# Performance work log

Hardware: AMD Instinct MI355X
Metric: run time of the kernel (lower is better)

Reference implementation:

```python
import jax, jax.numpy as jnp
import numpy as np

B, D, H, T = 2048, 16, 256, 50
BETA_MIN, BETA_MAX = 0.1, 20.0


def setup_inputs() -> dict:
    key = jax.random.key(0)
    ks = jax.random.split(key, 6)
    s1 = 1.0 / np.sqrt(D)
    s2 = 1.0 / np.sqrt(H)
    return {
        "x": jax.random.normal(ks[0], (B, D), dtype=jnp.float32),
        "W1": jax.random.normal(ks[1], (D, H), dtype=jnp.float32) * s1,
        "b1": jnp.zeros((H,), dtype=jnp.float32),
        "wt": jax.random.normal(ks[2], (H,), dtype=jnp.float32) * 0.1,
        "W2": jax.random.normal(ks[3], (H, D), dtype=jnp.float32) * s2,
        "b2": jnp.zeros((D,), dtype=jnp.float32),
    }


def _dynamics(x, t, W1, b1, wt, W2, b2):
    # Reverse-time probability-flow ODE drift for a VP-SDE:
    #   dx/dt = f(x,t) - 0.5 * g(t)^2 * score(x,t)
    # with f = -0.5*beta(t)*x, g^2 = beta(t), score = MLP(x, t).
    beta = BETA_MIN + t * (BETA_MAX - BETA_MIN)
    h = jnp.tanh(x @ W1 + t * wt + b1)  # [B, H]
    score = h @ W2 + b2                 # [B, D]
    return -0.5 * beta * (x + score)


def _trace_jac(f, x):
    # Exact per-sample trace of the [D, D] Jacobian of f (batched over B)
    # via D forward-mode JVPs with basis tangents (batched, no per-output loop).
    eye = jnp.eye(x.shape[-1], dtype=x.dtype)

    def jvp_col(e):
        _, jv = jax.jvp(f, (x,), (jnp.broadcast_to(e, x.shape),))
        return jv  # [B, D]

    cols = jax.vmap(jvp_col)(eye)       # [D, B, D]
    return jnp.einsum("ibi->b", cols)   # sum of Jacobian diagonal per sample


def reference(x, W1, b1, wt, W2, b2):
    times = jnp.linspace(1e-3, 1.0, T, dtype=jnp.float32)

    def F(xc, t):
        dyn = lambda y: _dynamics(y, t, W1, b1, wt, W2, b2)
        dx = dyn(xc)
        tr = _trace_jac(dyn, xc)
        return dx, tr

    def rk4_step(carry, ts):
        xc, ldj = carry
        t0, t1 = ts
        h = t1 - t0
        k1x, k1t = F(xc, t0)
        k2x, k2t = F(xc + 0.5 * h * k1x, t0 + 0.5 * h)
        k3x, k3t = F(xc + 0.5 * h * k2x, t0 + 0.5 * h)
        k4x, k4t = F(xc + h * k3x, t1)
        xn = xc + (h / 6.0) * (k1x + 2.0 * k2x + 2.0 * k3x + k4x)
        ln = ldj + (h / 6.0) * (k1t + 2.0 * k2t + 2.0 * k3t + k4t)
        return (xn, ln), (xn, ln)

    ldj0 = jnp.zeros((x.shape[0],), dtype=x.dtype)
    (xf, ldjf), (xs, _) = jax.lax.scan(
        rk4_step, (x, ldj0), (times[:-1], times[1:])
    )
    xt = jnp.concatenate([x[None], xs], axis=0)  # [T, B, D] trajectory
    return xf, ldjf, xt
```

## Files before the change

### kernel.cpp

```cpp
#include <hip/hip_runtime.h>
#include <stdint.h>


typedef _Float16 f16x2 __attribute__((ext_vector_type(2)));

#if defined(__has_builtin)
#if __has_builtin(__builtin_amdgcn_fdot2)
#define HAVE_FDOT2 1
#endif
#endif

__device__ __forceinline__ float fdot2f(f16x2 a, f16x2 b, float c) {
#ifdef HAVE_FDOT2
    return __builtin_amdgcn_fdot2(a, b, c, false);
#else
    return fmaf((float)a.y, (float)b.y, fmaf((float)a.x, (float)b.x, c));
#endif
}

__device__ __forceinline__ uint32_t pk(float a, float b) {
    f16x2 v; v.x = (_Float16)a; v.y = (_Float16)b;
    return __builtin_bit_cast(uint32_t, v);
}
__device__ __forceinline__ f16x2 upk(uint32_t u) {
    return __builtin_bit_cast(f16x2, u);
}

#define DPP_XOR1 0xB1
#define DPP_XOR2 0x4E
#define DPP_RHM  0x141
template <int CTRL>
__device__ __forceinline__ float dpp_add(float x) {
    int v = __builtin_amdgcn_update_dpp(
        0, __builtin_bit_cast(int, x), CTRL, 0xF, 0xF, true);
    return x + __builtin_bit_cast(float, v);
}

#define Bn 2048
#define Dn 16
#define Hn 256
#define Tn 50
#define CH 20

__global__ __launch_bounds__(64) void ode_kernel(
    const float* __restrict__ x_in,
    const float* __restrict__ W1,
    const float* __restrict__ b1v,
    const float* __restrict__ wtv,
    const float* __restrict__ W2,
    const float* __restrict__ b2v,
    float* __restrict__ out)
{
    __shared__ __align__(16) uint32_t h_lds[8 * CH];

    const int L  = threadIdx.x;
    const int g8 = L >> 3;
    const int c  = L & 7;
    const int ia = 2 * g8, ib = ia + 1;
    const int k0 = 4 * L;
    const int gs = blockIdx.x;

    const float K2 = 2.88539008f;

    f16x2 w1p[4][8];
    float b1k[4], wtk[4], ck[4];
    #pragma unroll
    for (int q = 0; q < 4; ++q) {
        const int k = k0 + q;
        #pragma unroll
        for (int j = 0; j < 8; ++j) {
            f16x2 v;
            v.x = (_Float16)(K2 * W1[(2 * j)     * Hn + k]);
            v.y = (_Float16)(K2 * W1[(2 * j + 1) * Hn + k]);
            w1p[q][j] = v;
        }
        b1k[q] = K2 * b1v[k];
        wtk[q] = K2 * wtv[k];
        float s = 0.f;
        #pragma unroll
        for (int ii = 0; ii < 16; ++ii)
            s = fmaf(W1[ii * Hn + k], W2[k * Dn + ii], s);
        ck[q] = s;
    }
    f16x2 w2a[16], w2b[16];
    #pragma unroll
    for (int m = 0; m < 16; ++m) {
        f16x2 va, vb;
        va.x = (_Float16)W2[(32 * c + 2 * m)     * Dn + ia];
        va.y = (_Float16)W2[(32 * c + 2 * m + 1) * Dn + ia];
        vb.x = (_Float16)W2[(32 * c + 2 * m)     * Dn + ib];
        vb.y = (_Float16)W2[(32 * c + 2 * m + 1) * Dn + ib];
        w2a[m] = va; w2b[m] = vb;
    }
    const float b2a = b2v[ia], b2b = b2v[ib];

    float xa = x_in[gs * Dn + ia];
    float xb = x_in[gs * Dn + ib];
    float ldjl  = 0.f;
    float wbsum = 0.f;

    float* xf_out  = out;
    float* ldj_out = out + (size_t)Bn * Dn;
    float* xt_ptr  = out + (size_t)Bn * Dn + Bn + gs * Dn + ia;

    if (c == 0) *(float2*)xt_ptr = make_float2(xa, xb);
    xt_ptr += Bn * Dn;

    const int hwidx = CH * (L >> 3) + 2 * (L & 7);

    uint32_t se0, se1, se2, se3, se4, se5, se6, se7;
    auto bcast = [&](float ea, float eb) {
        const uint32_t vpk = pk(ea, eb);
        se0 = __builtin_amdgcn_readlane(vpk,  0);
        se1 = __builtin_amdgcn_readlane(vpk,  8);
        se2 = __builtin_amdgcn_readlane(vpk, 16);
        se3 = __builtin_amdgcn_readlane(vpk, 24);
        se4 = __builtin_amdgcn_readlane(vpk, 32);
        se5 = __builtin_amdgcn_readlane(vpk, 40);
        se6 = __builtin_amdgcn_readlane(vpk, 48);
        se7 = __builtin_amdgcn_readlane(vpk, 56);
    };

    auto Feval = [&](float xeva, float xevb, float tt, float wgt,
                     float& dxa, float& dxb) {
        const f16x2 xp[8] = { upk(se0), upk(se1), upk(se2), upk(se3),
                              upk(se4), upk(se5), upk(se6), upk(se7) };
        float u0 = fmaf(tt, wtk[0], b1k[0]);
        float u1 = fmaf(tt, wtk[1], b1k[1]);
        float u2 = fmaf(tt, wtk[2], b1k[2]);
        float u3 = fmaf(tt, wtk[3], b1k[3]);
        #pragma unroll
        for (int j = 0; j < 8; ++j) {
            u0 = fdot2f(xp[j], w1p[0][j], u0);
            u1 = fdot2f(xp[j], w1p[1][j], u1);
            u2 = fdot2f(xp[j], w1p[2][j], u2);
            u3 = fdot2f(xp[j], w1p[3][j], u3);
        }
        const float h0 = fmaf(-2.f, __builtin_amdgcn_rcpf(__builtin_amdgcn_exp2f(u0) + 1.f), 1.f);
        const float h1 = fmaf(-2.f, __builtin_amdgcn_rcpf(__builtin_amdgcn_exp2f(u1) + 1.f), 1.f);
        const float h2 = fmaf(-2.f, __builtin_amdgcn_rcpf(__builtin_amdgcn_exp2f(u2) + 1.f), 1.f);
        const float h3 = fmaf(-2.f, __builtin_amdgcn_rcpf(__builtin_amdgcn_exp2f(u3) + 1.f), 1.f);
        *(uint2*)&h_lds[hwidx] = make_uint2(pk(h0, h1), pk(h2, h3));

        const float gl = (fmaf(-h0 * h0, ck[0], ck[0]) + fmaf(-h1 * h1, ck[1], ck[1]))
                       + (fmaf(-h2 * h2, ck[2], ck[2]) + fmaf(-h3 * h3, ck[3], ck[3]));
        const float beta = fmaf(tt, 19.9f, 0.1f);
        const float nhb  = -0.5f * beta;
        const float wb   = wgt * nhb;
        ldjl  = fmaf(wb, gl, ldjl);
        wbsum += wb;

        asm volatile("" ::: "memory");

        float sa0 = 0.f, sa1 = 0.f, sb0 = 0.f, sb1 = 0.f;
        #pragma unroll
        for (int mq = 0; mq < 4; ++mq) {
            const uint4 hv = *(const uint4*)&h_lds[CH * c + 4 * mq];
            const f16x2 p0 = upk(hv.x), p1 = upk(hv.y), p2 = upk(hv.z), p3 = upk(hv.w);
            sa0 = fdot2f(p0, w2a[4 * mq + 0], sa0);
            sb0 = fdot2f(p0, w2b[4 * mq + 0], sb0);
            sa1 = fdot2f(p1, w2a[4 * mq + 1], sa1);
            sb1 = fdot2f(p1, w2b[4 * mq + 1], sb1);
            sa0 = fdot2f(p2, w2a[4 * mq + 2], sa0);
            sb0 = fdot2f(p2, w2b[4 * mq + 2], sb0);
            sa1 = fdot2f(p3, w2a[4 * mq + 3], sa1);
            sb1 = fdot2f(p3, w2b[4 * mq + 3], sb1);
        }
        float sca = sa0 + sa1, scb = sb0 + sb1;
        sca = dpp_add<DPP_XOR1>(sca);  scb = dpp_add<DPP_XOR1>(scb);
        sca = dpp_add<DPP_XOR2>(sca);  scb = dpp_add<DPP_XOR2>(scb);
        sca = dpp_add<DPP_RHM >(sca);  scb = dpp_add<DPP_RHM >(scb);
        sca += b2a;  scb += b2b;

        dxa = nhb * (xeva + sca);
        dxb = nhb * (xevb + scb);
    };

    const float t_lo = 1e-3f;
    const float dt   = (1.0f - 1e-3f) / (float)(Tn - 1);
    const float hh   = dt;
    const float w1w  = hh * (1.f / 6.f);
    const float w2w  = hh * (2.f / 6.f);

    bcast(xa, xb);
    for (int j = 0; j < Tn - 1; ++j) {
        const float t0 = fmaf((float)j, dt, t_lo);
        const float tm = t0 + 0.5f * hh;
        const float t1 = t0 + hh;
        float k1a, k1b, k2a, k2b, k3a, k3b, k4a, k4b;

        Feval(xa, xb, t0, w1w, k1a, k1b);
        const float e2a = fmaf(0.5f * hh, k1a, xa);
        const float e2b = fmaf(0.5f * hh, k1b, xb);
        bcast(e2a, e2b);
        Feval(e2a, e2b, tm, w2w, k2a, k2b);
        const float e3a = fmaf(0.5f * hh, k2a, xa);
        const float e3b = fmaf(0.5f * hh, k2b, xb);
        bcast(e3a, e3b);
        Feval(e3a, e3b, tm, w2w, k3a, k3b);
        const float e4a = fmaf(hh, k3a, xa);
        const float e4b = fmaf(hh, k3b, xb);
        bcast(e4a, e4b);
        Feval(e4a, e4b, t1, w1w, k4a, k4b);

        xa = fmaf(w1w, k1a + 2.f * (k2a + k3a) + k4a, xa);
        xb = fmaf(w1w, k1b + 2.f * (k2b + k3b) + k4b, xb);
        if (c == 0) *(float2*)xt_ptr = make_float2(xa, xb);
        xt_ptr += Bn * Dn;
        bcast(xa, xb);
    }

    if (c == 0) *(float2*)(xf_out + gs * Dn + ia) = make_float2(xa, xb);

    ldjl = fmaf(0.25f, wbsum, ldjl);
    #pragma unroll
    for (int off = 1; off < 64; off <<= 1)
        ldjl += __shfl_xor(ldjl, off);
    if (L == 0) ldj_out[gs] = ldjl;
}

extern "C" void kernel_launch(void* const* d_in, const int* in_sizes, int n_in,
                              void* d_out, int out_size, void* d_ws, size_t ws_size,
                              hipStream_t stream) {
    const float* x  = (const float*)d_in[0];
    const float* W1 = (const float*)d_in[1];
    const float* b1 = (const float*)d_in[2];
    const float* wt = (const float*)d_in[3];
    const float* W2 = (const float*)d_in[4];
    const float* b2 = (const float*)d_in[5];
    (void)in_sizes; (void)n_in; (void)out_size; (void)d_ws; (void)ws_size;
    ode_kernel<<<Bn, 64, 0, stream>>>(x, W1, b1, wt, W2, b2, (float*)d_out);
}
```

Before: 171.6 us.

## Switch fp16 dot2 math to packed fp32 FMA with 4-output-per-lane layout

Replaces the fp16 fdot2 arithmetic for both MLP layers with packed fp32 v_pk_fma operations. Hidden activations are now kept in LDS as fp32. The second-layer work is remapped so each lane owns 4 output dims over 16 hidden chunks instead of 2 dims over 8 chunks, which needs one extra DPP reduction stage. This improves accuracy but doubles LDS traffic and register footprint, and packed fp32 FMA may give lower throughput than fp16 dot2 on this latency-bound, one-wave-per-sample kernel.

```diff
diff --git a/kernel.cpp b/kernel.cpp
--- a/kernel.cpp
+++ b/kernel.cpp
@@ -2,38 +2,26 @@
 #include <stdint.h>
 
 
-typedef _Float16 f16x2 __attribute__((ext_vector_type(2)));
-
-#if defined(__has_builtin)
-#if __has_builtin(__builtin_amdgcn_fdot2)
-#define HAVE_FDOT2 1
-#endif
-#endif
-
-__device__ __forceinline__ float fdot2f(f16x2 a, f16x2 b, float c) {
-#ifdef HAVE_FDOT2
-    return __builtin_amdgcn_fdot2(a, b, c, false);
-#else
-    return fmaf((float)a.y, (float)b.y, fmaf((float)a.x, (float)b.x, c));
-#endif
-}
-
-__device__ __forceinline__ uint32_t pk(float a, float b) {
-    f16x2 v; v.x = (_Float16)a; v.y = (_Float16)b;
-    return __builtin_bit_cast(uint32_t, v);
-}
-__device__ __forceinline__ f16x2 upk(uint32_t u) {
-    return __builtin_bit_cast(f16x2, u);
-}
-
-#define DPP_XOR1 0xB1
-#define DPP_XOR2 0x4E
-#define DPP_RHM  0x141
+typedef float v2f __attribute__((ext_vector_type(2)));
+
+__device__ __forceinline__ v2f fma2(v2f a, v2f b, v2f c) {
+    return __builtin_elementwise_fma(a, b, c);
+}
+
+#define DPP_X1  0xB1
+#define DPP_X2  0x4E
+#define DPP_HM  0x141
+#define DPP_MIR 0x140
 template <int CTRL>
 __device__ __forceinline__ float dpp_add(float x) {
-    int v = __builtin_amdgcn_update_dpp(
-        0, __builtin_bit_cast(int, x), CTRL, 0xF, 0xF, true);
+    const int xi = __builtin_bit_cast(int, x);
+    const int v  = __builtin_amdgcn_update_dpp(xi, xi, CTRL, 0xF, 0xF, false);
     return x + __builtin_bit_cast(float, v);
+}
+
+__device__ __forceinline__ float rlf(float v, int l) {
+    return __builtin_bit_cast(
+        float, __builtin_amdgcn_readlane(__builtin_bit_cast(int, v), l));
 }
 
 #define Bn 2048
@@ -51,28 +39,28 @@
     const float* __restrict__ b2v,
     float* __restrict__ out)
 {
-    __shared__ __align__(16) uint32_t h_lds[8 * CH];
+    __shared__ __align__(16) float h_lds[16 * CH];
 
     const int L  = threadIdx.x;
-    const int g8 = L >> 3;
-    const int c  = L & 7;
-    const int ia = 2 * g8, ib = ia + 1;
+    const int iq = L >> 4;
+    const int c4 = L & 15;
+    const int i0 = 4 * iq;
     const int k0 = 4 * L;
     const int gs = blockIdx.x;
 
     const float K2 = 2.88539008f;
 
-    f16x2 w1p[4][8];
+    v2f w1v[4][8];
     float b1k[4], wtk[4], ck[4];
     #pragma unroll
     for (int q = 0; q < 4; ++q) {
         const int k = k0 + q;
         #pragma unroll
         for (int j = 0; j < 8; ++j) {
-            f16x2 v;
-            v.x = (_Float16)(K2 * W1[(2 * j)     * Hn + k]);
-            v.y = (_Float16)(K2 * W1[(2 * j + 1) * Hn + k]);
-            w1p[q][j] = v;
+            v2f v;
+            v.x = K2 * W1[(2 * j)     * Hn + k];
+            v.y = K2 * W1[(2 * j + 1) * Hn + k];
+            w1v[q][j] = v;
         }
         b1k[q] = K2 * b1v[k];
         wtk[q] = K2 * wtv[k];
@@ -82,65 +70,62 @@
             s = fmaf(W1[ii * Hn + k], W2[k * Dn + ii], s);
         ck[q] = s;
     }
-    f16x2 w2a[16], w2b[16];
-    #pragma unroll
-    for (int m = 0; m < 16; ++m) {
-        f16x2 va, vb;
-        va.x = (_Float16)W2[(32 * c + 2 * m)     * Dn + ia];
-        va.y = (_Float16)W2[(32 * c + 2 * m + 1) * Dn + ia];
-        vb.x = (_Float16)W2[(32 * c + 2 * m)     * Dn + ib];
-        vb.y = (_Float16)W2[(32 * c + 2 * m + 1) * Dn + ib];
-        w2a[m] = va; w2b[m] = vb;
-    }
-    const float b2a = b2v[ia], b2b = b2v[ib];
-
-    float xa = x_in[gs * Dn + ia];
-    float xb = x_in[gs * Dn + ib];
-    float ldjl  = 0.f;
-    float wbsum = 0.f;
+    v2f w2v[4][8];
+    #pragma unroll
+    for (int q = 0; q < 4; ++q)
+        #pragma unroll
+        for (int n = 0; n < 8; ++n) {
+            v2f v;
+            v.x = W2[(16 * c4 + 2 * n)     * Dn + i0 + q];
+            v.y = W2[(16 * c4 + 2 * n + 1) * Dn + i0 + q];
+            w2v[q][n] = v;
+        }
+    float b2q[4];
+    #pragma unroll
+    for (int q = 0; q < 4; ++q) b2q[q] = b2v[i0 + q];
+
+    const float4 xld = *(const float4*)(x_in + gs * Dn + i0);
+    float x0 = xld.x, x1 = xld.y, x2 = xld.z, x3 = xld.w;
+    float ldjl = 0.f, wbsum = 0.f;
 
     float* xf_out  = out;
     float* ldj_out = out + (size_t)Bn * Dn;
-    float* xt_ptr  = out + (size_t)Bn * Dn + Bn + gs * Dn + ia;
-
-    if (c == 0) *(float2*)xt_ptr = make_float2(xa, xb);
+    float* xt_ptr  = out + (size_t)Bn * Dn + Bn + gs * Dn + i0;
+
+    if (c4 == 0) *(float4*)xt_ptr = make_float4(x0, x1, x2, x3);
     xt_ptr += Bn * Dn;
 
-    const int hwidx = CH * (L >> 3) + 2 * (L & 7);
-
-    uint32_t se0, se1, se2, se3, se4, se5, se6, se7;
-    auto bcast = [&](float ea, float eb) {
-        const uint32_t vpk = pk(ea, eb);
-        se0 = __builtin_amdgcn_readlane(vpk,  0);
-        se1 = __builtin_amdgcn_readlane(vpk,  8);
-        se2 = __builtin_amdgcn_readlane(vpk, 16);
-        se3 = __builtin_amdgcn_readlane(vpk, 24);
-        se4 = __builtin_amdgcn_readlane(vpk, 32);
-        se5 = __builtin_amdgcn_readlane(vpk, 40);
-        se6 = __builtin_amdgcn_readlane(vpk, 48);
-        se7 = __builtin_amdgcn_readlane(vpk, 56);
+    v2f xv[8];
+    auto bcast = [&](float e0, float e1, float e2, float e3) {
+        #pragma unroll
+        for (int j = 0; j < 4; ++j) {
+            v2f a, b;
+            a.x = rlf(e0, 16 * j);  a.y = rlf(e1, 16 * j);
+            b.x = rlf(e2, 16 * j);  b.y = rlf(e3, 16 * j);
+            xv[2 * j]     = a;
+            xv[2 * j + 1] = b;
+        }
     };
 
-    auto Feval = [&](float xeva, float xevb, float tt, float wgt,
-                     float& dxa, float& dxb) {
-        const f16x2 xp[8] = { upk(se0), upk(se1), upk(se2), upk(se3),
-                              upk(se4), upk(se5), upk(se6), upk(se7) };
-        float u0 = fmaf(tt, wtk[0], b1k[0]);
-        float u1 = fmaf(tt, wtk[1], b1k[1]);
-        float u2 = fmaf(tt, wtk[2], b1k[2]);
-        float u3 = fmaf(tt, wtk[3], b1k[3]);
+    auto Feval = [&](float e0, float e1, float e2, float e3, float tt, float wgt,
+                     float& d0, float& d1, float& d2, float& d3) {
+        v2f a0 = {0.f, 0.f}, a1 = {0.f, 0.f}, a2 = {0.f, 0.f}, a3 = {0.f, 0.f};
         #pragma unroll
         for (int j = 0; j < 8; ++j) {
-            u0 = fdot2f(xp[j], w1p[0][j], u0);
-            u1 = fdot2f(xp[j], w1p[1][j], u1);
-            u2 = fdot2f(xp[j], w1p[2][j], u2);
-            u3 = fdot2f(xp[j], w1p[3][j], u3);
-        }
+            a0 = fma2(xv[j], w1v[0][j], a0);
+            a1 = fma2(xv[j], w1v[1][j], a1);
+            a2 = fma2(xv[j], w1v[2][j], a2);
+            a3 = fma2(xv[j], w1v[3][j], a3);
+        }
+        const float u0 = fmaf(tt, wtk[0], b1k[0]) + (a0.x + a0.y);
+        const float u1 = fmaf(tt, wtk[1], b1k[1]) + (a1.x + a1.y);
+        const float u2 = fmaf(tt, wtk[2], b1k[2]) + (a2.x + a2.y);
+        const float u3 = fmaf(tt, wtk[3], b1k[3]) + (a3.x + a3.y);
         const float h0 = fmaf(-2.f, __builtin_amdgcn_rcpf(__builtin_amdgcn_exp2f(u0) + 1.f), 1.f);
         const float h1 = fmaf(-2.f, __builtin_amdgcn_rcpf(__builtin_amdgcn_exp2f(u1) + 1.f), 1.f);
         const float h2 = fmaf(-2.f, __builtin_amdgcn_rcpf(__builtin_amdgcn_exp2f(u2) + 1.f), 1.f);
         const float h3 = fmaf(-2.f, __builtin_amdgcn_rcpf(__builtin_amdgcn_exp2f(u3) + 1.f), 1.f);
-        *(uint2*)&h_lds[hwidx] = make_uint2(pk(h0, h1), pk(h2, h3));
+        *(float4*)&h_lds[CH * (L >> 2) + 4 * (L & 3)] = make_float4(h0, h1, h2, h3);
 
         const float gl = (fmaf(-h0 * h0, ck[0], ck[0]) + fmaf(-h1 * h1, ck[1], ck[1]))
                        + (fmaf(-h2 * h2, ck[2], ck[2]) + fmaf(-h3 * h3, ck[3], ck[3]));
@@ -152,28 +137,33 @@
 
         asm volatile("" ::: "memory");
 
-        float sa0 = 0.f, sa1 = 0.f, sb0 = 0.f, sb1 = 0.f;
-        #pragma unroll
-        for (int mq = 0; mq < 4; ++mq) {
-            const uint4 hv = *(const uint4*)&h_lds[CH * c + 4 * mq];
-            const f16x2 p0 = upk(hv.x), p1 = upk(hv.y), p2 = upk(hv.z), p3 = upk(hv.w);
-            sa0 = fdot2f(p0, w2a[4 * mq + 0], sa0);
-            sb0 = fdot2f(p0, w2b[4 * mq + 0], sb0);
-            sa1 = fdot2f(p1, w2a[4 * mq + 1], sa1);
-            sb1 = fdot2f(p1, w2b[4 * mq + 1], sb1);
-            sa0 = fdot2f(p2, w2a[4 * mq + 2], sa0);
-            sb0 = fdot2f(p2, w2b[4 * mq + 2], sb0);
-            sa1 = fdot2f(p3, w2a[4 * mq + 3], sa1);
-            sb1 = fdot2f(p3, w2b[4 * mq + 3], sb1);
-        }
-        float sca = sa0 + sa1, scb = sb0 + sb1;
-        sca = dpp_add<DPP_XOR1>(sca);  scb = dpp_add<DPP_XOR1>(scb);
-        sca = dpp_add<DPP_XOR2>(sca);  scb = dpp_add<DPP_XOR2>(scb);
-        sca = dpp_add<DPP_RHM >(sca);  scb = dpp_add<DPP_RHM >(scb);
-        sca += b2a;  scb += b2b;
-
-        dxa = nhb * (xeva + sca);
-        dxb = nhb * (xevb + scb);
+        const float* hb = &h_lds[CH * c4];
+        v2f s0 = {0.f, 0.f}, s1 = {0.f, 0.f}, s2 = {0.f, 0.f}, s3 = {0.f, 0.f};
+        #pragma unroll
+        for (int m = 0; m < 4; ++m) {
+            const float4 hp = *(const float4*)(hb + 4 * m);
+            v2f hA; hA.x = hp.x; hA.y = hp.y;
+            v2f hB; hB.x = hp.z; hB.y = hp.w;
+            s0 = fma2(hA, w2v[0][2 * m], s0);  s0 = fma2(hB, w2v[0][2 * m + 1], s0);
+            s1 = fma2(hA, w2v[1][2 * m], s1);  s1 = fma2(hB, w2v[1][2 * m + 1], s1);
+            s2 = fma2(hA, w2v[2][2 * m], s2);  s2 = fma2(hB, w2v[2][2 * m + 1], s2);
+            s3 = fma2(hA, w2v[3][2 * m], s3);  s3 = fma2(hB, w2v[3][2 * m + 1], s3);
+        }
+        float t0 = s0.x + s0.y, t1 = s1.x + s1.y;
+        float t2 = s2.x + s2.y, t3 = s3.x + s3.y;
+        t0 = dpp_add<DPP_X1 >(t0); t1 = dpp_add<DPP_X1 >(t1);
+        t2 = dpp_add<DPP_X1 >(t2); t3 = dpp_add<DPP_X1 >(t3);
+        t0 = dpp_add<DPP_X2 >(t0); t1 = dpp_add<DPP_X2 >(t1);
+        t2 = dpp_add<DPP_X2 >(t2); t3 = dpp_add<DPP_X2 >(t3);
+        t0 = dpp_add<DPP_HM >(t0); t1 = dpp_add<DPP_HM >(t1);
+        t2 = dpp_add<DPP_HM >(t2); t3 = dpp_add<DPP_HM >(t3);
+        t0 = dpp_add<DPP_MIR>(t0); t1 = dpp_add<DPP_MIR>(t1);
+        t2 = dpp_add<DPP_MIR>(t2); t3 = dpp_add<DPP_MIR>(t3);
+
+        d0 = nhb * (e0 + t0 + b2q[0]);
+        d1 = nhb * (e1 + t1 + b2q[1]);
+        d2 = nhb * (e2 + t2 + b2q[2]);
+        d3 = nhb * (e3 + t3 + b2q[3]);
     };
 
     const float t_lo = 1e-3f;
@@ -182,35 +172,37 @@
     const float w1w  = hh * (1.f / 6.f);
     const float w2w  = hh * (2.f / 6.f);
 
-    bcast(xa, xb);
+    bcast(x0, x1, x2, x3);
     for (int j = 0; j < Tn - 1; ++j) {
         const float t0 = fmaf((float)j, dt, t_lo);
         const float tm = t0 + 0.5f * hh;
         const float t1 = t0 + hh;
-        float k1a, k1b, k2a, k2b, k3a, k3b, k4a, k4b;
-
-        Feval(xa, xb, t0, w1w, k1a, k1b);
-        const float e2a = fmaf(0.5f * hh, k1a, xa);
-        const float e2b = fmaf(0.5f * hh, k1b, xb);
-        bcast(e2a, e2b);
-        Feval(e2a, e2b, tm, w2w, k2a, k2b);
-        const float e3a = fmaf(0.5f * hh, k2a, xa);
-        const float e3b = fmaf(0.5f * hh, k2b, xb);
-        bcast(e3a, e3b);
-        Feval(e3a, e3b, tm, w2w, k3a, k3b);
-        const float e4a = fmaf(hh, k3a, xa);
-        const float e4b = fmaf(hh, k3b, xb);
-        bcast(e4a, e4b);
-        Feval(e4a, e4b, t1, w1w, k4a, k4b);
-
-        xa = fmaf(w1w, k1a + 2.f * (k2a + k3a) + k4a, xa);
-        xb = fmaf(w1w, k1b + 2.f * (k2b + k3b) + k4b, xb);
-        if (c == 0) *(float2*)xt_ptr = make_float2(xa, xb);
+        float k1[4], k2[4], k3[4], k4[4];
+
+        Feval(x0, x1, x2, x3, t0, w1w, k1[0], k1[1], k1[2], k1[3]);
+        float e0 = fmaf(0.5f * hh, k1[0], x0), e1 = fmaf(0.5f * hh, k1[1], x1);
+        float e2 = fmaf(0.5f * hh, k1[2], x2), e3 = fmaf(0.5f * hh, k1[3], x3);
+        bcast(e0, e1, e2, e3);
+        Feval(e0, e1, e2, e3, tm, w2w, k2[0], k2[1], k2[2], k2[3]);
+        e0 = fmaf(0.5f * hh, k2[0], x0); e1 = fmaf(0.5f * hh, k2[1], x1);
+        e2 = fmaf(0.5f * hh, k2[2], x2); e3 = fmaf(0.5f * hh, k2[3], x3);
+        bcast(e0, e1, e2, e3);
+        Feval(e0, e1, e2, e3, tm, w2w, k3[0], k3[1], k3[2], k3[3]);
+        e0 = fmaf(hh, k3[0], x0); e1 = fmaf(hh, k3[1], x1);
+        e2 = fmaf(hh, k3[2], x2); e3 = fmaf(hh, k3[3], x3);
+        bcast(e0, e1, e2, e3);
+        Feval(e0, e1, e2, e3, t1, w1w, k4[0], k4[1], k4[2], k4[3]);
+
+        x0 = fmaf(w1w, k1[0] + 2.f * (k2[0] + k3[0]) + k4[0], x0);
+        x1 = fmaf(w1w, k1[1] + 2.f * (k2[1] + k3[1]) + k4[1], x1);
+        x2 = fmaf(w1w, k1[2] + 2.f * (k2[2] + k3[2]) + k4[2], x2);
+        x3 = fmaf(w1w, k1[3] + 2.f * (k2[3] + k3[3]) + k4[3], x3);
+        if (c4 == 0) *(float4*)xt_ptr = make_float4(x0, x1, x2, x3);
         xt_ptr += Bn * Dn;
-        bcast(xa, xb);
+        bcast(x0, x1, x2, x3);
     }
 
-    if (c == 0) *(float2*)(xf_out + gs * Dn + ia) = make_float2(xa, xb);
+    if (c4 == 0) *(float4*)(xf_out + gs * Dn + i0) = make_float4(x0, x1, x2, x3);
 
     ldjl = fmaf(0.25f, wbsum, ldjl);
     #pragma unroll
```

Measured after the change: 208.0 us. +21.2%, slower.

## Split each sample's hidden dimension across two wavefronts with LDS exchange

Applied to the files above, without the earlier changes.

Each block now uses 128 threads (two wavefronts) per sample instead of one. Each wave handles half of the 256 hidden units, which halves the per-thread W1/W2 register footprint and the fdot2 work. Partial score sums are exchanged through a double-buffered LDS array with a __syncthreads per function evaluation. The DPP reduction also changes to keep the old value on invalid lanes. In exchange the latency-bound serial chain gains 200 block barriers and extra LDS traffic, while total wave count doubles to 4096.

```diff
diff --git a/kernel.cpp b/kernel.cpp
--- a/kernel.cpp
+++ b/kernel.cpp
@@ -26,13 +26,13 @@
     return __builtin_bit_cast(f16x2, u);
 }
 
-#define DPP_XOR1 0xB1
-#define DPP_XOR2 0x4E
-#define DPP_RHM  0x141
+#define DPP_X1  0xB1
+#define DPP_X2  0x4E
+#define DPP_HM  0x141
 template <int CTRL>
 __device__ __forceinline__ float dpp_add(float x) {
-    int v = __builtin_amdgcn_update_dpp(
-        0, __builtin_bit_cast(int, x), CTRL, 0xF, 0xF, true);
+    const int xi = __builtin_bit_cast(int, x);
+    const int v  = __builtin_amdgcn_update_dpp(xi, xi, CTRL, 0xF, 0xF, false);
     return x + __builtin_bit_cast(float, v);
 }
 
@@ -40,9 +40,8 @@
 #define Dn 16
 #define Hn 256
 #define Tn 50
-#define CH 20
-
-__global__ __launch_bounds__(64) void ode_kernel(
+
+__global__ __launch_bounds__(128, 4) void ode_kernel(
     const float* __restrict__ x_in,
     const float* __restrict__ W1,
     const float* __restrict__ b1v,
@@ -51,22 +50,26 @@
     const float* __restrict__ b2v,
     float* __restrict__ out)
 {
-    __shared__ __align__(16) uint32_t h_lds[8 * CH];
-
-    const int L  = threadIdx.x;
+    __shared__ uint32_t h_lds[128];
+    __shared__ float    sc_buf[2][2][16];
+    __shared__ float    ldj_buf[2];
+
+    const int t  = threadIdx.x;
+    const int W  = t >> 6;
+    const int L  = t & 63;
     const int g8 = L >> 3;
     const int c  = L & 7;
     const int ia = 2 * g8, ib = ia + 1;
-    const int k0 = 4 * L;
+    const int kp = 64 * W + L;
     const int gs = blockIdx.x;
 
     const float K2 = 2.88539008f;
 
-    f16x2 w1p[4][8];
-    float b1k[4], wtk[4], ck[4];
+    f16x2 w1p[2][8];
+    float b1k[2], wtk[2], ck[2];
     #pragma unroll
-    for (int q = 0; q < 4; ++q) {
-        const int k = k0 + q;
+    for (int q = 0; q < 2; ++q) {
+        const int k = 2 * kp + q;
         #pragma unroll
         for (int j = 0; j < 8; ++j) {
             f16x2 v;
@@ -82,31 +85,30 @@
             s = fmaf(W1[ii * Hn + k], W2[k * Dn + ii], s);
         ck[q] = s;
     }
-    f16x2 w2a[16], w2b[16];
+    f16x2 w2a[8], w2b[8];
     #pragma unroll
-    for (int m = 0; m < 16; ++m) {
+    for (int m = 0; m < 8; ++m) {
+        const int kk = 128 * W + 16 * c + 2 * m;
         f16x2 va, vb;
-        va.x = (_Float16)W2[(32 * c + 2 * m)     * Dn + ia];
-        va.y = (_Float16)W2[(32 * c + 2 * m + 1) * Dn + ia];
-        vb.x = (_Float16)W2[(32 * c + 2 * m)     * Dn + ib];
-        vb.y = (_Float16)W2[(32 * c + 2 * m + 1) * Dn + ib];
+        va.x = (_Float16)W2[kk * Dn + ia];  va.y = (_Float16)W2[(kk + 1) * Dn + ia];
+        vb.x = (_Float16)W2[kk * Dn + ib];  vb.y = (_Float16)W2[(kk + 1) * Dn + ib];
         w2a[m] = va; w2b[m] = vb;
     }
     const float b2a = b2v[ia], b2b = b2v[ib];
 
     float xa = x_in[gs * Dn + ia];
     float xb = x_in[gs * Dn + ib];
-    float ldjl  = 0.f;
-    float wbsum = 0.f;
+    float ldjl = 0.f, wbsum = 0.f;
 
     float* xf_out  = out;
     float* ldj_out = out + (size_t)Bn * Dn;
     float* xt_ptr  = out + (size_t)Bn * Dn + Bn + gs * Dn + ia;
 
-    if (c == 0) *(float2*)xt_ptr = make_float2(xa, xb);
+    if (W == 0 && c == 0) *(float2*)xt_ptr = make_float2(xa, xb);
     xt_ptr += Bn * Dn;
 
-    const int hwidx = CH * (L >> 3) + 2 * (L & 7);
+    const int hwr = 64 * W + L;
+    const int hrd = 64 * W + 8 * c;
 
     uint32_t se0, se1, se2, se3, se4, se5, se6, se7;
     auto bcast = [&](float ea, float eb) {
@@ -121,29 +123,31 @@
         se7 = __builtin_amdgcn_readlane(vpk, 56);
     };
 
+    int fe = 0;
+
     auto Feval = [&](float xeva, float xevb, float tt, float wgt,
                      float& dxa, float& dxb) {
-        const f16x2 xp[8] = { upk(se0), upk(se1), upk(se2), upk(se3),
-                              upk(se4), upk(se5), upk(se6), upk(se7) };
+        const int p = fe & 1; ++fe;
+
         float u0 = fmaf(tt, wtk[0], b1k[0]);
         float u1 = fmaf(tt, wtk[1], b1k[1]);
-        float u2 = fmaf(tt, wtk[2], b1k[2]);
-        float u3 = fmaf(tt, wtk[3], b1k[3]);
-        #pragma unroll
-        for (int j = 0; j < 8; ++j) {
-            u0 = fdot2f(xp[j], w1p[0][j], u0);
-            u1 = fdot2f(xp[j], w1p[1][j], u1);
-            u2 = fdot2f(xp[j], w1p[2][j], u2);
-            u3 = fdot2f(xp[j], w1p[3][j], u3);
+        {
+            const f16x2 xp0 = upk(se0), xp1 = upk(se1), xp2 = upk(se2), xp3 = upk(se3);
+            const f16x2 xp4 = upk(se4), xp5 = upk(se5), xp6 = upk(se6), xp7 = upk(se7);
+            u0 = fdot2f(xp0, w1p[0][0], u0);  u1 = fdot2f(xp0, w1p[1][0], u1);
+            u0 = fdot2f(xp1, w1p[0][1], u0);  u1 = fdot2f(xp1, w1p[1][1], u1);
+            u0 = fdot2f(xp2, w1p[0][2], u0);  u1 = fdot2f(xp2, w1p[1][2], u1);
+            u0 = fdot2f(xp3, w1p[0][3], u0);  u1 = fdot2f(xp3, w1p[1][3], u1);
+            u0 = fdot2f(xp4, w1p[0][4], u0);  u1 = fdot2f(xp4, w1p[1][4], u1);
+            u0 = fdot2f(xp5, w1p[0][5], u0);  u1 = fdot2f(xp5, w1p[1][5], u1);
+            u0 = fdot2f(xp6, w1p[0][6], u0);  u1 = fdot2f(xp6, w1p[1][6], u1);
+            u0 = fdot2f(xp7, w1p[0][7], u0);  u1 = fdot2f(xp7, w1p[1][7], u1);
         }
         const float h0 = fmaf(-2.f, __builtin_amdgcn_rcpf(__builtin_amdgcn_exp2f(u0) + 1.f), 1.f);
         const float h1 = fmaf(-2.f, __builtin_amdgcn_rcpf(__builtin_amdgcn_exp2f(u1) + 1.f), 1.f);
-        const float h2 = fmaf(-2.f, __builtin_amdgcn_rcpf(__builtin_amdgcn_exp2f(u2) + 1.f), 1.f);
-        const float h3 = fmaf(-2.f, __builtin_amdgcn_rcpf(__builtin_amdgcn_exp2f(u3) + 1.f), 1.f);
-        *(uint2*)&h_lds[hwidx] = make_uint2(pk(h0, h1), pk(h2, h3));
-
-        const float gl = (fmaf(-h0 * h0, ck[0], ck[0]) + fmaf(-h1 * h1, ck[1], ck[1]))
-                       + (fmaf(-h2 * h2, ck[2], ck[2]) + fmaf(-h3 * h3, ck[3], ck[3]));
+        h_lds[hwr] = pk(h0, h1);
+
+        const float gl   = fmaf(-h0 * h0, ck[0], ck[0]) + fmaf(-h1 * h1, ck[1], ck[1]);
         const float beta = fmaf(tt, 19.9f, 0.1f);
         const float nhb  = -0.5f * beta;
         const float wb   = wgt * nhb;
@@ -152,28 +156,29 @@
 
         asm volatile("" ::: "memory");
 
-        float sa0 = 0.f, sa1 = 0.f, sb0 = 0.f, sb1 = 0.f;
-        #pragma unroll
-        for (int mq = 0; mq < 4; ++mq) {
-            const uint4 hv = *(const uint4*)&h_lds[CH * c + 4 * mq];
-            const f16x2 p0 = upk(hv.x), p1 = upk(hv.y), p2 = upk(hv.z), p3 = upk(hv.w);
-            sa0 = fdot2f(p0, w2a[4 * mq + 0], sa0);
-            sb0 = fdot2f(p0, w2b[4 * mq + 0], sb0);
-            sa1 = fdot2f(p1, w2a[4 * mq + 1], sa1);
-            sb1 = fdot2f(p1, w2b[4 * mq + 1], sb1);
-            sa0 = fdot2f(p2, w2a[4 * mq + 2], sa0);
-            sb0 = fdot2f(p2, w2b[4 * mq + 2], sb0);
-            sa1 = fdot2f(p3, w2a[4 * mq + 3], sa1);
-            sb1 = fdot2f(p3, w2b[4 * mq + 3], sb1);
-        }
-        float sca = sa0 + sa1, scb = sb0 + sb1;
-        sca = dpp_add<DPP_XOR1>(sca);  scb = dpp_add<DPP_XOR1>(scb);
-        sca = dpp_add<DPP_XOR2>(sca);  scb = dpp_add<DPP_XOR2>(scb);
-        sca = dpp_add<DPP_RHM >(sca);  scb = dpp_add<DPP_RHM >(scb);
-        sca += b2a;  scb += b2b;
-
-        dxa = nhb * (xeva + sca);
-        dxb = nhb * (xevb + scb);
+        const uint4 hv0 = *(const uint4*)&h_lds[hrd];
+        const uint4 hv1 = *(const uint4*)&h_lds[hrd + 4];
+        const f16x2 p0 = upk(hv0.x), p1 = upk(hv0.y), p2 = upk(hv0.z), p3 = upk(hv0.w);
+        const f16x2 p4 = upk(hv1.x), p5 = upk(hv1.y), p6 = upk(hv1.z), p7 = upk(hv1.w);
+        float sa = 0.f, sb = 0.f;
+        sa = fdot2f(p0, w2a[0], sa);  sb = fdot2f(p0, w2b[0], sb);
+        sa = fdot2f(p1, w2a[1], sa);  sb = fdot2f(p1, w2b[1], sb);
+        sa = fdot2f(p2, w2a[2], sa);  sb = fdot2f(p2, w2b[2], sb);
+        sa = fdot2f(p3, w2a[3], sa);  sb = fdot2f(p3, w2b[3], sb);
+        sa = fdot2f(p4, w2a[4], sa);  sb = fdot2f(p4, w2b[4], sb);
+        sa = fdot2f(p5, w2a[5], sa);  sb = fdot2f(p5, w2b[5], sb);
+        sa = fdot2f(p6, w2a[6], sa);  sb = fdot2f(p6, w2b[6], sb);
+        sa = fdot2f(p7, w2a[7], sa);  sb = fdot2f(p7, w2b[7], sb);
+        sa = dpp_add<DPP_X1>(sa);  sb = dpp_add<DPP_X1>(sb);
+        sa = dpp_add<DPP_X2>(sa);  sb = dpp_add<DPP_X2>(sb);
+        sa = dpp_add<DPP_HM>(sa);  sb = dpp_add<DPP_HM>(sb);
+
+        if (c < 2) sc_buf[p][W][ia + c] = (c == 0) ? sa : sb;
+        __syncthreads();
+        const float2 o = *(const float2*)&sc_buf[p][1 - W][ia];
+
+        dxa = nhb * (xeva + sa + o.x + b2a);
+        dxb = nhb * (xevb + sb + o.y + b2b);
     };
 
     const float t_lo = 1e-3f;
@@ -205,18 +210,20 @@
 
         xa = fmaf(w1w, k1a + 2.f * (k2a + k3a) + k4a, xa);
         xb = fmaf(w1w, k1b + 2.f * (k2b + k3b) + k4b, xb);
-        if (c == 0) *(float2*)xt_ptr = make_float2(xa, xb);
+        if (W == 0 && c == 0) *(float2*)xt_ptr = make_float2(xa, xb);
         xt_ptr += Bn * Dn;
         bcast(xa, xb);
     }
 
-    if (c == 0) *(float2*)(xf_out + gs * Dn + ia) = make_float2(xa, xb);
-
-    ldjl = fmaf(0.25f, wbsum, ldjl);
+    if (W == 0 && c == 0) *(float2*)(xf_out + gs * Dn + ia) = make_float2(xa, xb);
+
+    ldjl = fmaf(0.125f, wbsum, ldjl);
     #pragma unroll
     for (int off = 1; off < 64; off <<= 1)
         ldjl += __shfl_xor(ldjl, off);
-    if (L == 0) ldj_out[gs] = ldjl;
+    if (L == 0) ldj_buf[W] = ldjl;
+    __syncthreads();
+    if (t == 0) ldj_out[gs] = ldj_buf[0] + ldj_buf[1];
 }
 
 extern "C" void kernel_launch(void* const* d_in, const int* in_sizes, int n_in,
@@ -229,5 +236,5 @@
     const float* W2 = (const float*)d_in[4];
     const float* b2 = (const float*)d_in[5];
     (void)in_sizes; (void)n_in; (void)out_size; (void)d_ws; (void)ws_size;
-    ode_kernel<<<Bn, 64, 0, stream>>>(x, W1, b1, wt, W2, b2, (float*)d_out);
-}
+    ode_kernel<<<Bn, 128, 0, stream>>>(x, W1, b1, wt, W2, b2, (float*)d_out);
+}
```

Result: slower. 218.5 us (+27.3%).
